# Performance work log

Hardware: AMD Instinct MI355X
Metric: run time of the kernel (lower is better)

Reference implementation:

```python
import jax, jax.numpy as jnp
import numpy as np

KERNEL_SIZE = 15  # matches init kwarg


def setup_inputs() -> dict:
    key = jax.random.key(0)
    k1, k2 = jax.random.split(key)
    B, T, C, H, W = 1, 8, 3, 96, 96
    K2 = KERNEL_SIZE * KERNEL_SIZE
    data = jax.random.normal(k1, (B, T, C, H, W), dtype=jnp.float32)
    kernels = jax.random.uniform(k2, (B, T, K2, C, H, W), dtype=jnp.float32)
    return {"data": data, "kernels": kernels}


def reference(data, kernels):
    # data:    [B, T, C, H, W]
    # kernels: [B, T, K*K, C, H, W]
    K = KERNEL_SIZE
    p = K // 2
    H, W = data.shape[-2], data.shape[-1]
    # zero-pad spatial dims (matches F.pad with default mode='constant')
    dp = jnp.pad(data, ((0, 0), (0, 0), (0, 0), (p, p), (p, p)))
    # shift-stack: tap order is i (row offset) major, j (col offset) minor,
    # matching the torch double loop.  stack axis=2 -> [B, T, K*K, C, H, W]
    img_stack = jnp.stack(
        [dp[..., i:i + H, j:j + W] for i in range(K) for j in range(K)],
        axis=2,
    )
    # per-pixel dynamic kernel: multiply and reduce over the K*K taps
    pred_burst = jnp.sum(kernels * img_stack, axis=2)  # [B, T, C, H, W]
    return pred_burst
```

## Files before the change

### kernel.cpp

```cpp
#include <hip/hip_runtime.h>


typedef float vf4 __attribute__((ext_vector_type(4)));

constexpr int K  = 15;
constexpr int P  = 7;
constexpr int H  = 96;
constexpr int W  = 96;
constexpr int C  = 3;
constexpr int T  = 8;
constexpr int HW = H * W;
constexpr int K2 = K * K;
constexpr int NP = T * C;
constexpr int NE = NP * HW;
constexpr size_t CHW = (size_t)C * HW;
constexpr int NQ   = NE / 4;
constexpr int BLK  = 64;
constexpr int NBLK = NQ / BLK;

__device__ __forceinline__ vf4 nt4(const float* p) {
    return __builtin_nontemporal_load(reinterpret_cast<const vf4*>(p));
}

__global__ __launch_bounds__(BLK) void kpn_fused_nt(
    const float* __restrict__ data,
    const float* __restrict__ kern,
    float* __restrict__ out)
{
    const int q     = blockIdx.x * BLK + threadIdx.x;
    const int w4    = q % (W / 4);
    const int rem   = q / (W / 4);
    const int h     = rem % H;
    const int plane = rem / H;
    const int t     = plane / C;
    const int c     = plane % C;
    const int col   = w4 * 4;

    const float* __restrict__ kbase =
        kern + ((size_t)(t * K2) * C + (size_t)c) * HW + (size_t)h * W + col;
    const float* __restrict__ dpl = data + plane * HW;

    int  colc[K + 3];
    bool cval[K + 3];
    #pragma unroll
    for (int m = 0; m < K + 3; ++m) {
        const int cc = col - P + m;
        cval[m] = (cc >= 0) && (cc < W);
        colc[m] = (cc < 0) ? 0 : ((cc >= W) ? (W - 1) : cc);
    }

    float acc[4] = {0.f, 0.f, 0.f, 0.f};

    auto load_row = [&](vf4 (&buf)[K], int i) {
        const float* p = kbase + (size_t)(i * K) * CHW;
        #pragma unroll
        for (int j = 0; j < K; ++j) buf[j] = nt4(p + (size_t)j * CHW);
    };

    auto consume_row = [&](vf4 (&buf)[K], int i) {
        const int srow = h + i - P;
        const bool rv  = (srow >= 0) && (srow < H);
        const float* __restrict__ drow = dpl + (rv ? srow : 0) * W;
        float dwin[K + 3];
        #pragma unroll
        for (int m = 0; m < K + 3; ++m) {
            const float v = drow[colc[m]];
            dwin[m] = (rv && cval[m]) ? v : 0.f;
        }
        #pragma unroll
        for (int j = 0; j < K; ++j) {
            acc[0] += buf[j][0] * dwin[j + 0];
            acc[1] += buf[j][1] * dwin[j + 1];
            acc[2] += buf[j][2] * dwin[j + 2];
            acc[3] += buf[j][3] * dwin[j + 3];
        }
    };

    vf4 A[K], B[K];
    load_row(A, 0);
    #pragma unroll 1
    for (int i = 0; i < K - 1; i += 2) {
        load_row(B, i + 1);
        consume_row(A, i);
        load_row(A, i + 2);
        consume_row(B, i + 1);
    }
    consume_row(A, K - 1);

    vf4 o = { acc[0], acc[1], acc[2], acc[3] };
    float* op = out + (size_t)plane * HW + (size_t)h * W + col;
    __builtin_nontemporal_store(o, reinterpret_cast<vf4*>(op));
}

extern "C" void kernel_launch(void* const* d_in, const int* in_sizes, int n_in,
                              void* d_out, int out_size, void* d_ws, size_t ws_size,
                              hipStream_t stream) {
    const float* data = (const float*)d_in[0];
    const float* kern = (const float*)d_in[1];
    float* out        = (float*)d_out;
    hipLaunchKernelGGL(kpn_fused_nt, dim3(NBLK), dim3(BLK), 0, stream,
                       data, kern, out);
}
```

Baseline: 277.4 us.

## Split the 15 kernel rows across four waves and reduce through shared memory

Each block now runs four waves that cover the same 64 output quads. Each wave handles up to four of the 15 tap rows, and the partial sums are combined in LDS after a barrier. This quadruples the memory-level parallelism per output, so more of the ~200MB streaming read of per-pixel kernels is in flight across the GPU. The cost is a shared-memory reduction, a __syncthreads, more total threads, and the data-window loads repeated in each wave.

```diff
diff --git a/kernel.cpp b/kernel.cpp
--- a/kernel.cpp
+++ b/kernel.cpp
@@ -15,19 +15,22 @@
 constexpr int NE = NP * HW;
 constexpr size_t CHW = (size_t)C * HW;
 constexpr int NQ   = NE / 4;
-constexpr int BLK  = 64;
-constexpr int NBLK = NQ / BLK;
+constexpr int QPB  = 64;
+constexpr int BLK  = 256;
+constexpr int NBLK = NQ / QPB;
 
 __device__ __forceinline__ vf4 nt4(const float* p) {
     return __builtin_nontemporal_load(reinterpret_cast<const vf4*>(p));
 }
 
-__global__ __launch_bounds__(BLK) void kpn_fused_nt(
+__global__ __launch_bounds__(BLK) void kpn_split4(
     const float* __restrict__ data,
     const float* __restrict__ kern,
     float* __restrict__ out)
 {
-    const int q     = blockIdx.x * BLK + threadIdx.x;
+    const int lane  = threadIdx.x & 63;
+    const int wave  = threadIdx.x >> 6;
+    const int q     = blockIdx.x * QPB + lane;
     const int w4    = q % (W / 4);
     const int rem   = q / (W / 4);
     const int h     = rem % H;
@@ -76,20 +79,37 @@
         }
     };
 
-    vf4 A[K], B[K];
-    load_row(A, 0);
-    #pragma unroll 1
-    for (int i = 0; i < K - 1; i += 2) {
-        load_row(B, i + 1);
-        consume_row(A, i);
-        load_row(A, i + 2);
-        consume_row(B, i + 1);
+    const int r0 = wave * 4;
+    vf4 A[K], Bv[K];
+    load_row(A, r0);
+    load_row(Bv, r0 + 1);
+    consume_row(A, r0);
+    load_row(A, r0 + 2);
+    consume_row(Bv, r0 + 1);
+    if (wave != 3) load_row(Bv, r0 + 3);
+    consume_row(A, r0 + 2);
+    if (wave != 3) consume_row(Bv, r0 + 3);
+
+    __shared__ float red[3][4][QPB];
+    if (wave != 0) {
+        red[wave - 1][0][lane] = acc[0];
+        red[wave - 1][1][lane] = acc[1];
+        red[wave - 1][2][lane] = acc[2];
+        red[wave - 1][3][lane] = acc[3];
     }
-    consume_row(A, K - 1);
-
-    vf4 o = { acc[0], acc[1], acc[2], acc[3] };
-    float* op = out + (size_t)plane * HW + (size_t)h * W + col;
-    __builtin_nontemporal_store(o, reinterpret_cast<vf4*>(op));
+    __syncthreads();
+    if (wave == 0) {
+        #pragma unroll
+        for (int wv = 0; wv < 3; ++wv) {
+            acc[0] += red[wv][0][lane];
+            acc[1] += red[wv][1][lane];
+            acc[2] += red[wv][2][lane];
+            acc[3] += red[wv][3][lane];
+        }
+        vf4 o = { acc[0], acc[1], acc[2], acc[3] };
+        float* op = out + (size_t)plane * HW + (size_t)h * W + col;
+        __builtin_nontemporal_store(o, reinterpret_cast<vf4*>(op));
+    }
 }
 
 extern "C" void kernel_launch(void* const* d_in, const int* in_sizes, int n_in,
@@ -98,6 +118,6 @@
     const float* data = (const float*)d_in[0];
     const float* kern = (const float*)d_in[1];
     float* out        = (float*)d_out;
-    hipLaunchKernelGGL(kpn_fused_nt, dim3(NBLK), dim3(BLK), 0, stream,
+    hipLaunchKernelGGL(kpn_split4, dim3(NBLK), dim3(BLK), 0, stream,
                        data, kern, out);
 }
```

Result: no change. 281.7 us (+1.5%).
